# Kernel tuning notes

Hardware: AMD Instinct MI355X
Metric: run time of the kernel (lower is better)

Reference implementation:

```python
import jax, jax.numpy as jnp
import numpy as np

N_LAYERS = 4
HID = 64
N_NODES = 50000
N_EDGES = 800000
N_GRAPHS = 256
NUM_ATOM = 100
NUM_BOND = 4
BN_EPS = 1e-5
GATE_EPS = 1e-6


def _batch_norm(x, gamma, beta):
    # training-mode BatchNorm1d over the node/edge dimension
    mu = jnp.mean(x, axis=0)
    var = jnp.var(x, axis=0)
    return gamma * (x - mu) * jax.lax.rsqrt(var + BN_EPS) + beta


def setup_inputs() -> dict:
    key = jax.random.key(0)
    ks = jax.random.split(key, 12)
    h = jax.random.randint(ks[0], (N_NODES,), 0, NUM_ATOM)
    e = jax.random.randint(ks[1], (N_EDGES,), 0, NUM_BOND)
    src = jax.random.randint(ks[2], (N_EDGES,), 0, N_NODES)
    dst = jax.random.randint(ks[3], (N_EDGES,), 0, N_NODES)
    graph_ids = jnp.sort(jax.random.randint(ks[4], (N_NODES,), 0, N_GRAPHS))
    node_emb = jax.random.normal(ks[5], (NUM_ATOM, HID), dtype=jnp.float32) * 0.1
    edge_emb = jax.random.normal(ks[6], (NUM_BOND, HID), dtype=jnp.float32) * 0.1
    bn_h_gamma = jnp.ones((N_LAYERS, HID), jnp.float32)
    bn_h_beta = jnp.zeros((N_LAYERS, HID), jnp.float32)
    bn_e_gamma = jnp.ones((N_LAYERS, HID), jnp.float32)
    bn_e_beta = jnp.zeros((N_LAYERS, HID), jnp.float32)
    W1 = jax.random.normal(ks[7], (HID, HID // 2), dtype=jnp.float32) * (1.0 / np.sqrt(HID))
    b1 = jnp.zeros((HID // 2,), jnp.float32)
    W2 = jax.random.normal(ks[8], (HID // 2, HID // 4), dtype=jnp.float32) * (1.0 / np.sqrt(HID // 2))
    b2 = jnp.zeros((HID // 4,), jnp.float32)
    W3 = jax.random.normal(ks[9], (HID // 4, 1), dtype=jnp.float32) * (1.0 / np.sqrt(HID // 4))
    b3 = jnp.zeros((1,), jnp.float32)
    return {"h": h, "e": e, "src": src, "dst": dst, "graph_ids": graph_ids,
            "node_emb": node_emb, "edge_emb": edge_emb,
            "bn_h_gamma": bn_h_gamma, "bn_h_beta": bn_h_beta,
            "bn_e_gamma": bn_e_gamma, "bn_e_beta": bn_e_beta,
            "W1": W1, "b1": b1, "W2": W2, "b2": b2, "W3": W3, "b3": b3}


def reference(h, e, src, dst, graph_ids, node_emb, edge_emb,
              bn_h_gamma, bn_h_beta, bn_e_gamma, bn_e_beta,
              W1, b1, W2, b2, W3, b3):
    hf = node_emb[h]          # [N, HID] node encoder
    ef = edge_emb[e]          # [E, HID] edge encoder
    ones_e = jnp.ones((N_EDGES,), hf.dtype)
    deg = jax.ops.segment_sum(ones_e, dst, num_segments=N_NODES)
    norm = jax.lax.rsqrt(jnp.maximum(deg, 1.0))[:, None]  # deg^-0.5, clamp(min=1)
    for l in range(N_LAYERS):
        h_in, e_in = hf, ef
        e_new = hf[src] + hf[dst] + ef            # gather: edge gate pre-activation
        sigma = jax.nn.sigmoid(e_new)
        hn = hf * norm
        msg = jax.ops.segment_sum(sigma * hn[src], dst, num_segments=N_NODES)
        den = jax.ops.segment_sum(sigma, dst, num_segments=N_NODES)
        h_new = (hn + msg / (den + GATE_EPS)) * norm
        h_new = _batch_norm(h_new, bn_h_gamma[l], bn_h_beta[l])
        e_new = _batch_norm(e_new, bn_e_gamma[l], bn_e_beta[l])
        hf = h_in + jax.nn.relu(h_new)            # residual
        ef = e_in + jax.nn.relu(e_new)
    # per-graph mean pooling (dgl.mean_nodes over the batched graph)
    ones_n = jnp.ones((N_NODES,), hf.dtype)
    counts = jax.ops.segment_sum(ones_n, graph_ids, num_segments=N_GRAPHS)
    hg = jax.ops.segment_sum(hf, graph_ids, num_segments=N_GRAPHS)
    hg = hg / jnp.maximum(counts, 1.0)[:, None]   # [G, HID]
    x = jax.nn.relu(hg @ W1 + b1)
    x = jax.nn.relu(x @ W2 + b2)
    return x @ W3 + b3                            # [G, 1]
```

## Files before the change

kernel.cpp:

```cpp
#include <hip/hip_runtime.h>
#include <math.h>

#define N_NODES 50000
#define N_EDGES 800000
#define HID 64
#define N_GRAPHS 256
#define BN_EPS 1e-5f
#define GATE_EPS 1e-6f

static inline size_t align256(size_t x) { return (x + 255) & ~(size_t)255; }


__global__ void k_zero(int* __restrict__ p, int n) {
    for (int i = blockIdx.x * blockDim.x + threadIdx.x; i < n; i += gridDim.x * blockDim.x)
        p[i] = 0;
}

__global__ void k_deg(const int* __restrict__ dst, int* __restrict__ deg) {
    for (int i = blockIdx.x * blockDim.x + threadIdx.x; i < N_EDGES; i += gridDim.x * blockDim.x)
        atomicAdd(&deg[dst[i]], 1);
}

__global__ void k_norm(const int* __restrict__ deg, float* __restrict__ norm) {
    int i = blockIdx.x * blockDim.x + threadIdx.x;
    if (i < N_NODES) norm[i] = 1.0f / sqrtf(fmaxf((float)deg[i], 1.0f));
}

__global__ void k_scan1(const int* __restrict__ deg, int* __restrict__ start,
                        int* __restrict__ blksum) {
    __shared__ int s[256];
    int t = threadIdx.x;
    int i = blockIdx.x * 256 + t;
    int v = (i < N_NODES) ? deg[i] : 0;
    s[t] = v;
    __syncthreads();
    for (int off = 1; off < 256; off <<= 1) {
        int x = (t >= off) ? s[t - off] : 0;
        __syncthreads();
        s[t] += x;
        __syncthreads();
    }
    if (i < N_NODES) start[i] = s[t] - v;
    if (t == 255) blksum[blockIdx.x] = s[255];
}

__global__ void k_scan2(int* __restrict__ blksum, int nb) {
    __shared__ int s[256];
    int t = threadIdx.x;
    int v = (t < nb) ? blksum[t] : 0;
    s[t] = v;
    __syncthreads();
    for (int off = 1; off < 256; off <<= 1) {
        int x = (t >= off) ? s[t - off] : 0;
        __syncthreads();
        s[t] += x;
        __syncthreads();
    }
    if (t < nb) blksum[t] = s[t] - v;
}

__global__ void k_scan3(int* __restrict__ start, const int* __restrict__ blksum,
                        int* __restrict__ cursor) {
    int i = blockIdx.x * 256 + threadIdx.x;
    if (i < N_NODES) {
        int v = start[i] + blksum[blockIdx.x];
        start[i] = v;
        cursor[i] = v;
    }
    if (blockIdx.x == 0 && threadIdx.x == 0) start[N_NODES] = N_EDGES;
}

__global__ void k_scatter(const int* __restrict__ dst, const int* __restrict__ src,
                          const int* __restrict__ etype, const float* __restrict__ norm,
                          int* __restrict__ cursor, int2* __restrict__ edge_meta) {
    for (int i = blockIdx.x * blockDim.x + threadIdx.x; i < N_EDGES; i += gridDim.x * blockDim.x) {
        int p = atomicAdd(&cursor[dst[i]], 1);
        int s = src[i];
        edge_meta[p] = make_int2(s | (etype[i] << 24), __float_as_int(norm[s]));
    }
}

__global__ __launch_bounds__(256) void k_embed(const int* __restrict__ h,
                                               const float* __restrict__ node_emb,
                                               float4* __restrict__ pair4) {
    const int total2 = N_NODES * (HID / 2);
    for (int i = blockIdx.x * blockDim.x + threadIdx.x; i < total2; i += gridDim.x * blockDim.x) {
        int n = i >> 5, c2 = i & 31;
        float2 e = ((const float2*)node_emb)[h[n] * (HID / 2) + c2];
        pair4[i] = make_float4(e.x, 0.f, e.y, 0.f);
    }
}

template <int MODE>
__global__ __launch_bounds__(256, 4) void k_edge(
    const int* __restrict__ start, const int2* __restrict__ edge_meta,
    const float* __restrict__ edge_emb,
    float* __restrict__ ef,
    const float2* __restrict__ pair,
    const float* __restrict__ norm, float* __restrict__ h_new,
    const float* __restrict__ stats_prev, const float* __restrict__ gamma_prev,
    const float* __restrict__ beta_prev,
    float* __restrict__ stats_e_out, float* __restrict__ stats_h_out) {
    const int lane = threadIdx.x & 63;
    const int wid = __builtin_amdgcn_readfirstlane(blockIdx.x * 4 + (threadIdx.x >> 6));
    const int n0 = wid * 4;

    __shared__ float s_emb[4 * HID];
    if (MODE <= 1) {
        for (int i = threadIdx.x; i < 4 * HID; i += blockDim.x) s_emb[i] = edge_emb[i];
        __syncthreads();
    }
    float a_prev = 0.f, c_prev = 0.f;
    if (MODE >= 1) {
        float s1 = stats_prev[lane], s2 = stats_prev[HID + lane];
        float mu = s1 * (1.0f / N_EDGES);
        float var = s2 * (1.0f / N_EDGES) - mu * mu;
        float rstd = 1.0f / sqrtf(var + BN_EPS);
        a_prev = gamma_prev[lane] * rstd;
        c_prev = beta_prev[lane] - mu * a_prev;
    }

    int jbeg[4], len[4];
    float hnn[4], hon[4], amsg[4], aden[4];
    int maxlen = 0;
#pragma unroll
    for (int k = 0; k < 4; ++k) {
        jbeg[k] = __builtin_amdgcn_readfirstlane(start[n0 + k]);
        len[k] = __builtin_amdgcn_readfirstlane(start[n0 + k + 1]) - jbeg[k];
        maxlen = max(maxlen, len[k]);
        float2 o = pair[(size_t)(n0 + k) * HID + lane];
        hnn[k] = o.x;
        hon[k] = (MODE >= 1) ? o.y : 0.f;
        amsg[k] = 0.f;
        aden[k] = 0.f;
    }

    auto eslot = [&](int k, int it) {
        int itc = min(it, max(len[k] - 1, 0));
        return min(jbeg[k] + itc, N_EDGES - 1);
    };

    float sum_e = 0.f, sumsq_e = 0.f, sum_h = 0.f, sumsq_h = 0.f;
    if (maxlen > 0) {
        int2 mt0[4], mt1[4];
        float ef0[4], ef1[4];
        float2 hp0[4];
#pragma unroll
        for (int k = 0; k < 4; ++k) {
            const int j = eslot(k, 0);
            mt0[k] = edge_meta[j];
            ef0[k] = (MODE >= 2) ? ef[(size_t)j * HID + lane] : 0.f;
        }
#pragma unroll
        for (int k = 0; k < 4; ++k)
            hp0[k] = pair[(size_t)(mt0[k].x & 0xFFFFFF) * HID + lane];
#pragma unroll
        for (int k = 0; k < 4; ++k) {
            const int j = eslot(k, 1);
            mt1[k] = edge_meta[j];
            ef1[k] = (MODE >= 2) ? ef[(size_t)j * HID + lane] : 0.f;
        }
        for (int it = 0; it < maxlen; ++it) {
            float2 hp1[4];
#pragma unroll
            for (int k = 0; k < 4; ++k)
                hp1[k] = pair[(size_t)(mt1[k].x & 0xFFFFFF) * HID + lane];
            int2 mt2[4];
            float ef2[4];
            const int itn = (it + 2 < maxlen) ? it + 2 : maxlen - 1;
#pragma unroll
            for (int k = 0; k < 4; ++k) {
                const int j = eslot(k, itn);
                mt2[k] = edge_meta[j];
                ef2[k] = (MODE >= 2) ? ef[(size_t)j * HID + lane] : 0.f;
            }
            __builtin_amdgcn_sched_barrier(0);
#pragma unroll
            for (int k = 0; k < 4; ++k) {
                const bool act = it < len[k];
                float efv;
                if (MODE == 0) {
                    efv = s_emb[(mt0[k].x >> 24) * HID + lane];
                } else if (MODE == 1) {
                    const float e0v = s_emb[(mt0[k].x >> 24) * HID + lane];
                    const float ep = hp0[k].y + hon[k] + e0v;
                    efv = e0v + fmaxf(a_prev * ep + c_prev, 0.f);
                    if (act) ef[(size_t)(jbeg[k] + it) * HID + lane] = efv;
                } else {
                    const float ep = hp0[k].y + hon[k] + ef0[k];
                    efv = ef0[k] + fmaxf(a_prev * ep + c_prev, 0.f);
                    if (MODE == 2) {
                        if (act) ef[(size_t)(jbeg[k] + it) * HID + lane] = efv;
                    }
                }
                const float en = hp0[k].x + hnn[k] + efv;
                const float sgm = 1.0f / (1.0f + __expf(-en));
                if (act) {
                    amsg[k] += sgm * hp0[k].x * __int_as_float(mt0[k].y);
                    aden[k] += sgm;
                    if (MODE != 3) { sum_e += en; sumsq_e += en * en; }
                }
            }
#pragma unroll
            for (int k = 0; k < 4; ++k) {
                mt0[k] = mt1[k]; ef0[k] = ef1[k]; hp0[k] = hp1[k];
                mt1[k] = mt2[k]; ef1[k] = ef2[k];
            }
        }
    }

#pragma unroll
    for (int k = 0; k < 4; ++k) {
        const float nm = norm[n0 + k];
        const float hval = (hnn[k] * nm + amsg[k] / (aden[k] + GATE_EPS)) * nm;
        h_new[(n0 + k) * HID + lane] = hval;
        sum_h += hval;
        sumsq_h += hval * hval;
    }

    __shared__ float sred[4][256];
    sred[0][threadIdx.x] = sum_e;
    sred[1][threadIdx.x] = sumsq_e;
    sred[2][threadIdx.x] = sum_h;
    sred[3][threadIdx.x] = sumsq_h;
    __syncthreads();
    if (threadIdx.x < 64) {
        const int t = threadIdx.x;
        if (MODE != 3) {
            float t1 = sred[0][t] + sred[0][t + 64] + sred[0][t + 128] + sred[0][t + 192];
            float t2 = sred[1][t] + sred[1][t + 64] + sred[1][t + 128] + sred[1][t + 192];
            atomicAdd(&stats_e_out[t], t1);
            atomicAdd(&stats_e_out[HID + t], t2);
        }
        float t3 = sred[2][t] + sred[2][t + 64] + sred[2][t + 128] + sred[2][t + 192];
        float t4 = sred[3][t] + sred[3][t + 64] + sred[3][t + 128] + sred[3][t + 192];
        atomicAdd(&stats_h_out[t], t3);
        atomicAdd(&stats_h_out[HID + t], t4);
    }
}

__global__ __launch_bounds__(256) void k_hupd(
    float4* pair4, const float2* __restrict__ h_new2,
    const float* __restrict__ stats, const float* __restrict__ gamma,
    const float* __restrict__ beta) {
    const int tid = blockIdx.x * blockDim.x + threadIdx.x;
    const int cb = (tid & 31) * 2;
    float a[2], c[2];
#pragma unroll
    for (int k = 0; k < 2; ++k) {
        int ch = cb + k;
        float mu = stats[ch] * (1.0f / N_NODES);
        float var = stats[HID + ch] * (1.0f / N_NODES) - mu * mu;
        float rstd = 1.0f / sqrtf(var + BN_EPS);
        a[k] = gamma[ch] * rstd;
        c[k] = beta[ch] - mu * a[k];
    }
    const int total2 = N_NODES * (HID / 2);
    for (int i = tid; i < total2; i += gridDim.x * blockDim.x) {
        float4 p = pair4[i];
        float2 hn = h_new2[i];
        float o0 = p.x + fmaxf(a[0] * hn.x + c[0], 0.f);
        float o1 = p.z + fmaxf(a[1] * hn.y + c[1], 0.f);
        pair4[i] = make_float4(o0, p.x, o1, p.z);
    }
}

__global__ __launch_bounds__(256) void k_poolmlp(
    const float2* __restrict__ pair, const int* __restrict__ graph_ids,
    const float* __restrict__ W1, const float* __restrict__ b1,
    const float* __restrict__ W2, const float* __restrict__ b2,
    const float* __restrict__ W3, const float* __restrict__ b3,
    float* __restrict__ out) {
    const int g = blockIdx.x;
    int a = 0, b = N_NODES;
    while (a < b) { int m = (a + b) >> 1; if (graph_ids[m] < g) a = m + 1; else b = m; }
    const int lo = a;
    b = N_NODES;
    while (a < b) { int m = (a + b) >> 1; if (graph_ids[m] < g + 1) a = m + 1; else b = m; }
    const int hi = a;

    const int lane = threadIdx.x & 63, w = threadIdx.x >> 6;
    float acc = 0.f;
    for (int n = lo + w; n < hi; n += 4) acc += pair[(size_t)n * HID + lane].x;
    __shared__ float sred[256];
    __shared__ float sh[64], sx1[32], sx2[16];
    sred[threadIdx.x] = acc;
    __syncthreads();
    if (threadIdx.x < 64) {
        float tot = sred[lane] + sred[lane + 64] + sred[lane + 128] + sred[lane + 192];
        sh[lane] = tot / fmaxf((float)(hi - lo), 1.0f);
    }
    __syncthreads();
    const int t = threadIdx.x;
    if (t < 32) {
        float s = b1[t];
        for (int c = 0; c < 64; ++c) s += sh[c] * W1[c * 32 + t];
        sx1[t] = fmaxf(s, 0.f);
    }
    __syncthreads();
    if (t < 16) {
        float s = b2[t];
        for (int k = 0; k < 32; ++k) s += sx1[k] * W2[k * 16 + t];
        sx2[t] = fmaxf(s, 0.f);
    }
    __syncthreads();
    if (t == 0) {
        float s = b3[0];
        for (int k = 0; k < 16; ++k) s += sx2[k] * W3[k];
        out[g] = s;
    }
}


extern "C" void kernel_launch(void* const* d_in, const int* in_sizes, int n_in,
                              void* d_out, int out_size, void* d_ws, size_t ws_size,
                              hipStream_t stream) {
    const int* h_idx      = (const int*)d_in[0];
    const int* e_idx      = (const int*)d_in[1];
    const int* src        = (const int*)d_in[2];
    const int* dst        = (const int*)d_in[3];
    const int* graph_ids  = (const int*)d_in[4];
    const float* node_emb = (const float*)d_in[5];
    const float* edge_emb = (const float*)d_in[6];
    const float* bnh_g    = (const float*)d_in[7];
    const float* bnh_b    = (const float*)d_in[8];
    const float* bne_g    = (const float*)d_in[9];
    const float* bne_b    = (const float*)d_in[10];
    const float* W1       = (const float*)d_in[11];
    const float* b1       = (const float*)d_in[12];
    const float* W2       = (const float*)d_in[13];
    const float* b2       = (const float*)d_in[14];
    const float* W3       = (const float*)d_in[15];
    const float* b3       = (const float*)d_in[16];
    float* out = (float*)d_out;

    char* w = (char*)d_ws;
    size_t off = 0;
    auto alloc = [&](size_t bytes) -> void* {
        void* p = w + off;
        off = align256(off + bytes);
        return p;
    };
    float*  ef        = (float*)alloc((size_t)N_EDGES * HID * 4);
    float2* pair      = (float2*)alloc((size_t)N_NODES * HID * 8);
    float*  h_new     = (float*)alloc((size_t)N_NODES * HID * 4);
    float*  norm      = (float*)alloc((size_t)N_NODES * 4);
    int2*   edge_meta = (int2*)alloc((size_t)N_EDGES * 8);
    int*    start     = (int*)alloc((size_t)(N_NODES + 1) * 4);
    int*    cursor    = (int*)alloc((size_t)N_NODES * 4);
    int*    blksum    = (int*)alloc(256 * 4);
    size_t zoff = off;
    int*    deg       = (int*)alloc((size_t)N_NODES * 4);
    float*  stats_e   = (float*)alloc(4 * 2 * HID * 4);
    float*  stats_h   = (float*)alloc(4 * 2 * HID * 4);
    int zero_elems = (int)((off - zoff) / 4);
    int* zbase = (int*)(w + zoff);

    const int NB_SCAN = (N_NODES + 255) / 256;

    k_zero<<<64, 256, 0, stream>>>(zbase, zero_elems);
    k_deg<<<1024, 256, 0, stream>>>(dst, deg);
    k_norm<<<NB_SCAN, 256, 0, stream>>>(deg, norm);
    k_scan1<<<NB_SCAN, 256, 0, stream>>>(deg, start, blksum);
    k_scan2<<<1, 256, 0, stream>>>(blksum, NB_SCAN);
    k_scan3<<<NB_SCAN, 256, 0, stream>>>(start, blksum, cursor);
    k_scatter<<<1024, 256, 0, stream>>>(dst, src, e_idx, norm, cursor, edge_meta);
    k_embed<<<512, 256, 0, stream>>>(h_idx, node_emb, (float4*)pair);

    const int EG = N_NODES / 16;
    const int NG = 512;

    k_edge<0><<<EG, 256, 0, stream>>>(start, edge_meta, edge_emb, ef,
        pair, norm, h_new, nullptr, nullptr, nullptr,
        stats_e + 0 * 128, stats_h + 0 * 128);
    k_hupd<<<NG, 256, 0, stream>>>((float4*)pair, (const float2*)h_new,
        stats_h + 0 * 128, bnh_g + 0 * HID, bnh_b + 0 * HID);

    k_edge<1><<<EG, 256, 0, stream>>>(start, edge_meta, edge_emb, ef,
        pair, norm, h_new, stats_e + 0 * 128, bne_g + 0 * HID, bne_b + 0 * HID,
        stats_e + 1 * 128, stats_h + 1 * 128);
    k_hupd<<<NG, 256, 0, stream>>>((float4*)pair, (const float2*)h_new,
        stats_h + 1 * 128, bnh_g + 1 * HID, bnh_b + 1 * HID);

    k_edge<2><<<EG, 256, 0, stream>>>(start, edge_meta, edge_emb, ef,
        pair, norm, h_new, stats_e + 1 * 128, bne_g + 1 * HID, bne_b + 1 * HID,
        stats_e + 2 * 128, stats_h + 2 * 128);
    k_hupd<<<NG, 256, 0, stream>>>((float4*)pair, (const float2*)h_new,
        stats_h + 2 * 128, bnh_g + 2 * HID, bnh_b + 2 * HID);

    k_edge<3><<<EG, 256, 0, stream>>>(start, edge_meta, edge_emb, ef,
        pair, norm, h_new, stats_e + 2 * 128, bne_g + 2 * HID, bne_b + 2 * HID,
        stats_e + 3 * 128, stats_h + 3 * 128);
    k_hupd<<<NG, 256, 0, stream>>>((float4*)pair, (const float2*)h_new,
        stats_h + 3 * 128, bnh_g + 3 * HID, bnh_b + 3 * HID);

    k_poolmlp<<<N_GRAPHS, 256, 0, stream>>>(pair, graph_ids, W1, b1, W2, b2, W3, b3, out);
}
```

Before: 775.3 us.

## Sort destination nodes by in-degree to balance per-wave edge work

```diff
diff --git a/kernel.cpp b/kernel.cpp
--- a/kernel.cpp
+++ b/kernel.cpp
@@ -24,6 +24,24 @@
 __global__ void k_norm(const int* __restrict__ deg, float* __restrict__ norm) {
     int i = blockIdx.x * blockDim.x + threadIdx.x;
     if (i < N_NODES) norm[i] = 1.0f / sqrtf(fmaxf((float)deg[i], 1.0f));
+}
+
+__global__ void k_hist(const int* __restrict__ deg, int* __restrict__ bins) {
+    int i = blockIdx.x * blockDim.x + threadIdx.x;
+    if (i < N_NODES) atomicAdd(&bins[min(deg[i], 255)], 1);
+}
+
+__global__ void k_permscatter(const int* __restrict__ deg, int* __restrict__ bins,
+                              int* __restrict__ perm, int* __restrict__ rank_of,
+                              int* __restrict__ deg_rank) {
+    int i = blockIdx.x * blockDim.x + threadIdx.x;
+    if (i < N_NODES) {
+        int d = deg[i];
+        int r = atomicAdd(&bins[min(d, 255)], 1);
+        perm[r] = i;
+        rank_of[i] = r;
+        deg_rank[r] = d;
+    }
 }
 
 __global__ void k_scan1(const int* __restrict__ deg, int* __restrict__ start,
@@ -72,9 +90,10 @@
 
 __global__ void k_scatter(const int* __restrict__ dst, const int* __restrict__ src,
                           const int* __restrict__ etype, const float* __restrict__ norm,
+                          const int* __restrict__ rank_of,
                           int* __restrict__ cursor, int2* __restrict__ edge_meta) {
     for (int i = blockIdx.x * blockDim.x + threadIdx.x; i < N_EDGES; i += gridDim.x * blockDim.x) {
-        int p = atomicAdd(&cursor[dst[i]], 1);
+        int p = atomicAdd(&cursor[rank_of[dst[i]]], 1);
         int s = src[i];
         edge_meta[p] = make_int2(s | (etype[i] << 24), __float_as_int(norm[s]));
     }
@@ -93,7 +112,8 @@
 
 template <int MODE>
 __global__ __launch_bounds__(256, 4) void k_edge(
-    const int* __restrict__ start, const int2* __restrict__ edge_meta,
+    const int* __restrict__ start, const int* __restrict__ perm,
+    const int2* __restrict__ edge_meta,
     const float* __restrict__ edge_emb,
     float* __restrict__ ef,
     const float2* __restrict__ pair,
@@ -103,7 +123,7 @@
     float* __restrict__ stats_e_out, float* __restrict__ stats_h_out) {
     const int lane = threadIdx.x & 63;
     const int wid = __builtin_amdgcn_readfirstlane(blockIdx.x * 4 + (threadIdx.x >> 6));
-    const int n0 = wid * 4;
+    const int r0 = wid * 4;
 
     __shared__ float s_emb[4 * HID];
     if (MODE <= 1) {
@@ -120,15 +140,16 @@
         c_prev = beta_prev[lane] - mu * a_prev;
     }
 
-    int jbeg[4], len[4];
+    int nid[4], jbeg[4], len[4];
     float hnn[4], hon[4], amsg[4], aden[4];
     int maxlen = 0;
 #pragma unroll
     for (int k = 0; k < 4; ++k) {
-        jbeg[k] = __builtin_amdgcn_readfirstlane(start[n0 + k]);
-        len[k] = __builtin_amdgcn_readfirstlane(start[n0 + k + 1]) - jbeg[k];
+        nid[k] = __builtin_amdgcn_readfirstlane(perm[r0 + k]);
+        jbeg[k] = __builtin_amdgcn_readfirstlane(start[r0 + k]);
+        len[k] = __builtin_amdgcn_readfirstlane(start[r0 + k + 1]) - jbeg[k];
         maxlen = max(maxlen, len[k]);
-        float2 o = pair[(size_t)(n0 + k) * HID + lane];
+        float2 o = pair[(size_t)nid[k] * HID + lane];
         hnn[k] = o.x;
         hon[k] = (MODE >= 1) ? o.y : 0.f;
         amsg[k] = 0.f;
@@ -211,9 +232,9 @@
 
 #pragma unroll
     for (int k = 0; k < 4; ++k) {
-        const float nm = norm[n0 + k];
+        const float nm = norm[nid[k]];
         const float hval = (hnn[k] * nm + amsg[k] / (aden[k] + GATE_EPS)) * nm;
-        h_new[(n0 + k) * HID + lane] = hval;
+        h_new[(size_t)nid[k] * HID + lane] = hval;
         sum_h += hval;
         sumsq_h += hval * hval;
     }
@@ -349,8 +370,12 @@
     int*    start     = (int*)alloc((size_t)(N_NODES + 1) * 4);
     int*    cursor    = (int*)alloc((size_t)N_NODES * 4);
     int*    blksum    = (int*)alloc(256 * 4);
+    int*    perm      = (int*)alloc((size_t)N_NODES * 4);
+    int*    rank_of   = (int*)alloc((size_t)N_NODES * 4);
+    int*    deg_rank  = (int*)alloc((size_t)N_NODES * 4);
     size_t zoff = off;
     int*    deg       = (int*)alloc((size_t)N_NODES * 4);
+    int*    bins      = (int*)alloc(256 * 4);
     float*  stats_e   = (float*)alloc(4 * 2 * HID * 4);
     float*  stats_h   = (float*)alloc(4 * 2 * HID * 4);
     int zero_elems = (int)((off - zoff) / 4);
@@ -361,34 +386,37 @@
     k_zero<<<64, 256, 0, stream>>>(zbase, zero_elems);
     k_deg<<<1024, 256, 0, stream>>>(dst, deg);
     k_norm<<<NB_SCAN, 256, 0, stream>>>(deg, norm);
-    k_scan1<<<NB_SCAN, 256, 0, stream>>>(deg, start, blksum);
+    k_hist<<<NB_SCAN, 256, 0, stream>>>(deg, bins);
+    k_scan2<<<1, 256, 0, stream>>>(bins, 256);
+    k_permscatter<<<NB_SCAN, 256, 0, stream>>>(deg, bins, perm, rank_of, deg_rank);
+    k_scan1<<<NB_SCAN, 256, 0, stream>>>(deg_rank, start, blksum);
     k_scan2<<<1, 256, 0, stream>>>(blksum, NB_SCAN);
     k_scan3<<<NB_SCAN, 256, 0, stream>>>(start, blksum, cursor);
-    k_scatter<<<1024, 256, 0, stream>>>(dst, src, e_idx, norm, cursor, edge_meta);
+    k_scatter<<<1024, 256, 0, stream>>>(dst, src, e_idx, norm, rank_of, cursor, edge_meta);
     k_embed<<<512, 256, 0, stream>>>(h_idx, node_emb, (float4*)pair);
 
     const int EG = N_NODES / 16;
     const int NG = 512;
 
-    k_edge<0><<<EG, 256, 0, stream>>>(start, edge_meta, edge_emb, ef,
+    k_edge<0><<<EG, 256, 0, stream>>>(start, perm, edge_meta, edge_emb, ef,
         pair, norm, h_new, nullptr, nullptr, nullptr,
         stats_e + 0 * 128, stats_h + 0 * 128);
     k_hupd<<<NG, 256, 0, stream>>>((float4*)pair, (const float2*)h_new,
         stats_h + 0 * 128, bnh_g + 0 * HID, bnh_b + 0 * HID);
 
-    k_edge<1><<<EG, 256, 0, stream>>>(start, edge_meta, edge_emb, ef,
+    k_edge<1><<<EG, 256, 0, stream>>>(start, perm, edge_meta, edge_emb, ef,
         pair, norm, h_new, stats_e + 0 * 128, bne_g + 0 * HID, bne_b + 0 * HID,
         stats_e + 1 * 128, stats_h + 1 * 128);
     k_hupd<<<NG, 256, 0, stream>>>((float4*)pair, (const float2*)h_new,
         stats_h + 1 * 128, bnh_g + 1 * HID, bnh_b + 1 * HID);
 
-    k_edge<2><<<EG, 256, 0, stream>>>(start, edge_meta, edge_emb, ef,
+    k_edge<2><<<EG, 256, 0, stream>>>(start, perm, edge_meta, edge_emb, ef,
         pair, norm, h_new, stats_e + 1 * 128, bne_g + 1 * HID, bne_b + 1 * HID,
         stats_e + 2 * 128, stats_h + 2 * 128);
     k_hupd<<<NG, 256, 0, stream>>>((float4*)pair, (const float2*)h_new,
         stats_h + 2 * 128, bnh_g + 2 * HID, bnh_b + 2 * HID);
 
-    k_edge<3><<<EG, 256, 0, stream>>>(start, edge_meta, edge_emb, ef,
+    k_edge<3><<<EG, 256, 0, stream>>>(start, perm, edge_meta, edge_emb, ef,
         pair, norm, h_new, stats_e + 2 * 128, bne_g + 2 * HID, bne_b + 2 * HID,
         stats_e + 3 * 128, stats_h + 3 * 128);
     k_hupd<<<NG, 256, 0, stream>>>((float4*)pair, (const float2*)h_new,
```

Result: slower. 1.011 ms (+30.4%).
